# Optimization experiments

Hardware: AMD Instinct MI355X
Metric: run time of the kernel (lower is better)

Reference implementation:

```python
import jax, jax.numpy as jnp
import numpy as np

NUM_HEADS = 4
OUTPUT_DIM = 32
NUM_NODES = 50000
NUM_EDGES = 800000
INPUT_DIM = 128


def setup_inputs() -> dict:
    key = jax.random.key(0)
    k1, k2, k3, k4 = jax.random.split(key, 4)
    node_features = jax.random.uniform(k1, (NUM_NODES, INPUT_DIM), dtype=jnp.float32)
    edge_index = jax.random.randint(k2, (2, NUM_EDGES), 0, NUM_NODES, dtype=jnp.int64)
    # Linear weight (xavier-like scale), stored as [in, out] for x @ W
    W = jax.random.normal(k3, (INPUT_DIM, NUM_HEADS * OUTPUT_DIM), dtype=jnp.float32) * 0.1
    att = jax.random.normal(k4, (2 * OUTPUT_DIM, 1), dtype=jnp.float32) * 0.2
    return {"node_features": node_features, "edge_index": edge_index, "W": W, "att": att}


def reference(node_features, edge_index, W, att):
    num_nodes = node_features.shape[0]
    # Linear projection -> [N, H, D]  (dropout = identity in eval mode)
    proj = (node_features @ W).reshape(num_nodes, NUM_HEADS, OUTPUT_DIM)
    src = proj[edge_index[0]]   # [E, H, D]
    tgt = proj[edge_index[1]]   # [E, H, D]
    # concat([src,tgt]) @ att  ==  src @ att[:D] + tgt @ att[D:]
    a_src = att[:OUTPUT_DIM, 0]   # [D]
    a_tgt = att[OUTPUT_DIM:, 0]   # [D]
    scores = jax.nn.leaky_relu(
        jnp.einsum('ehd,d->eh', src, a_src) + jnp.einsum('ehd,d->eh', tgt, a_tgt),
        negative_slope=0.01,
    )  # [E, H]
    # Faithful to original: softmax over the HEADS axis (dim=-1 of [E, H])
    alpha = jax.nn.softmax(scores, axis=-1)  # [E, H]
    weighted = tgt * alpha[..., None]        # [E, H, D]
    # index_add_ on dim 0 with edge_index[0]
    out = jax.ops.segment_sum(weighted, edge_index[0], num_segments=num_nodes)  # [N, H, D]
    # concat_heads=False -> mean over heads
    return out.mean(axis=1)  # [N, D]
```

## Files before the change

kernel.cpp:

```cpp
#include <hip/hip_runtime.h>
#include <math.h>

#define N_NODES 50000
#define N_EDGES 800000
#define IN_DIM 128
#define N_HEADS 4
#define OUT_DIM 32
#define PROJ_DIM 128
#define WSTR 144

#define NBIN 196
#define BINCAP 5000
#define MAXDEG 64

#define PROJ_BLKS 391
#define PART_BLKS 391
#define FUSE_BLKS (NBIN + PROJ_BLKS)

typedef short bf16x8 __attribute__((ext_vector_type(8)));
typedef float f32x4  __attribute__((ext_vector_type(4)));
typedef _Float16 h2  __attribute__((ext_vector_type(2)));

__device__ __forceinline__ ushort f32_to_bf16(float f) {
    unsigned u = __float_as_uint(f);
    unsigned r = u + 0x7fffu + ((u >> 16) & 1u);
    return (ushort)(r >> 16);
}

__device__ __forceinline__ bf16x8 cvt8(float4 a, float4 b) {
    bf16x8 r;
    r[0] = (short)f32_to_bf16(a.x); r[1] = (short)f32_to_bf16(a.y);
    r[2] = (short)f32_to_bf16(a.z); r[3] = (short)f32_to_bf16(a.w);
    r[4] = (short)f32_to_bf16(b.x); r[5] = (short)f32_to_bf16(b.y);
    r[6] = (short)f32_to_bf16(b.z); r[7] = (short)f32_to_bf16(b.w);
    return r;
}

__device__ __forceinline__ ushort f32_to_f16(float f) {
    return __builtin_bit_cast(ushort, (_Float16)f);
}

__global__ __launch_bounds__(256) void partition_kernel(
    const int* __restrict__ ei, int* __restrict__ bin_cursor,
    unsigned* __restrict__ slab)
{
    __shared__ int cnt[256];
    __shared__ int gbase[256];

    const int tid = threadIdx.x;

    for (int t = tid; t < NBIN; t += 256) cnt[t] = 0;
    __syncthreads();

    const int ebase = blockIdx.x * 2048;
    unsigned srcv[8], tgtv[8];
    int rank[8];
#pragma unroll
    for (int i = 0; i < 8; ++i) {
        int e = ebase + i * 256 + tid;
        bool ok = e < N_EDGES;
        srcv[i] = ok ? (unsigned)ei[e] : 0u;
        tgtv[i] = ok ? (unsigned)ei[N_EDGES + e] : 0u;
        rank[i] = ok ? atomicAdd(&cnt[srcv[i] >> 8], 1) : -1;
    }
    __syncthreads();

    for (int t = tid; t < NBIN; t += 256)
        gbase[t] = atomicAdd(&bin_cursor[t], cnt[t]);
    __syncthreads();

#pragma unroll
    for (int i = 0; i < 8; ++i) {
        if (rank[i] >= 0) {
            int bin = srcv[i] >> 8;
            int p = gbase[bin] + rank[i];
            if (p < BINCAP)
                slab[bin * BINCAP + p] = (tgtv[i] << 16) | (srcv[i] & 255u);
        }
    }
}

__global__ __launch_bounds__(256) void fused_kernel(
    const float* __restrict__ X, const float* __restrict__ W,
    const float* __restrict__ att,
    const unsigned* __restrict__ slab, const int* __restrict__ bin_cursor,
    ushort* __restrict__ projT, float* __restrict__ s_src, float* __restrict__ s_tgt,
    ushort* __restrict__ csr, int* __restrict__ offs, int* __restrict__ deg)
{
    __shared__ ushort Wt[128 * WSTR];

    const int tid = threadIdx.x;

    if (blockIdx.x < NBIN) {
        int*    cnt2 = (int*)Wt;
        int*    ex   = cnt2 + 256;
        int*    wsum = ex + 256;
        ushort* stgt = (ushort*)(wsum + 8);

        const int b = blockIdx.x;
        const int t = tid;
        const int lane = t & 63;
        const int wid  = t >> 6;
        int n_e = bin_cursor[b];
        n_e = (n_e < BINCAP) ? n_e : BINCAP;

        cnt2[t] = 0;
        __syncthreads();

        unsigned pk[20];
        int npk = 0;
        for (int i = t; i < n_e; i += 256) {
            unsigned v = slab[b * BINCAP + i];
            int node8 = v & 255u;
            int r = atomicAdd(&cnt2[node8], 1);
            r = (r < 255) ? r : 255;
            pk[npk++] = (v & 0xFFFF0000u) | ((unsigned)r << 8) | (unsigned)node8;
        }
        __syncthreads();

        const int v = cnt2[t];
        int x = v;
#pragma unroll
        for (int off = 1; off < 64; off <<= 1) {
            int y = __shfl_up(x, off);
            x += (lane >= off) ? y : 0;
        }
        if (lane == 63) wsum[wid] = x;
        __syncthreads();
        int add = 0;
#pragma unroll
        for (int w = 0; w < 4; ++w) add += (w < wid) ? wsum[w] : 0;
        const int myex = x + add - v;
        const int mycnt = v;
        ex[t] = myex;
        __syncthreads();

        for (int j = 0; j < npk; ++j) {
            unsigned pv = pk[j];
            int lpos = ex[pv & 255u] + (int)((pv >> 8) & 255u);
            if (lpos < BINCAP) stgt[lpos] = (ushort)(pv >> 16);
        }
        __syncthreads();

        for (int i = t; i < n_e; i += 256) csr[b * BINCAP + i] = stgt[i];
        int node = b * 256 + t;
        if (node < N_NODES) {
            offs[node] = b * BINCAP + myex;
            deg[node]  = mycnt;
        }
        return;
    }

    for (int idx = tid; idx < 64 * 128; idx += 256) {
        int kp = idx >> 7;
        int c  = idx & 127;
        float w0 = W[(2 * kp) * PROJ_DIM + c];
        float w1 = W[(2 * kp + 1) * PROJ_DIM + c];
        unsigned pr = (unsigned)f32_to_bf16(w0) | ((unsigned)f32_to_bf16(w1) << 16);
        *(unsigned*)&Wt[c * WSTR + 2 * kp] = pr;
    }
    __syncthreads();

    const int wv   = tid >> 6;
    const int lane = tid & 63;
    const int m = lane & 15;
    const int q = lane >> 4;
    const int rbase = (blockIdx.x - NBIN) * 128;

    int arow0 = rbase + wv * 32 + m;
    int arow1 = arow0 + 16;
    arow0 = (arow0 < N_NODES) ? arow0 : N_NODES - 1;
    arow1 = (arow1 < N_NODES) ? arow1 : N_NODES - 1;
    const long long xb0 = (long long)arow0 * IN_DIM;
    const long long xb1 = (long long)arow1 * IN_DIM;

    f32x4 acc[2][8];
#pragma unroll
    for (int rt = 0; rt < 2; ++rt)
#pragma unroll
        for (int ct = 0; ct < 8; ++ct) acc[rt][ct] = (f32x4){0.f, 0.f, 0.f, 0.f};

#pragma unroll
    for (int ks = 0; ks < 4; ++ks) {
        const int k0 = ks * 32 + q * 8;
        float4 a0lo = *(const float4*)&X[xb0 + k0];
        float4 a0hi = *(const float4*)&X[xb0 + k0 + 4];
        float4 a1lo = *(const float4*)&X[xb1 + k0];
        float4 a1hi = *(const float4*)&X[xb1 + k0 + 4];
        bf16x8 afrag0 = cvt8(a0lo, a0hi);
        bf16x8 afrag1 = cvt8(a1lo, a1hi);
#pragma unroll
        for (int ct = 0; ct < 8; ++ct) {
            bf16x8 bfrag = *(const bf16x8*)&Wt[(ct * 16 + m) * WSTR + k0];
            acc[0][ct] = __builtin_amdgcn_mfma_f32_16x16x32_bf16(afrag0, bfrag, acc[0][ct], 0, 0, 0);
            acc[1][ct] = __builtin_amdgcn_mfma_f32_16x16x32_bf16(afrag1, bfrag, acc[1][ct], 0, 0, 0);
        }
    }

    const float as_lo = att[m],      as_hi = att[m + 16];
    const float at_lo = att[32 + m], at_hi = att[48 + m];

#pragma unroll
    for (int rt = 0; rt < 2; ++rt) {
        const int rowb = rbase + wv * 32 + rt * 16 + q * 4;
#pragma unroll
        for (int r = 0; r < 4; ++r) {
            const int row = rowb + r;
            float cl[4], ch[4];
#pragma unroll
            for (int h = 0; h < 4; ++h) {
                cl[h] = acc[rt][2 * h][r];
                ch[h] = acc[rt][2 * h + 1][r];
            }
            if (row < N_NODES) {
                ushort4 plo, phi;
                plo.x = f32_to_f16(cl[0]); plo.y = f32_to_f16(cl[1]);
                plo.z = f32_to_f16(cl[2]); plo.w = f32_to_f16(cl[3]);
                phi.x = f32_to_f16(ch[0]); phi.y = f32_to_f16(ch[1]);
                phi.z = f32_to_f16(ch[2]); phi.w = f32_to_f16(ch[3]);
                *(ushort4*)&projT[(long long)row * PROJ_DIM + m * 4] = plo;
                *(ushort4*)&projT[(long long)row * PROJ_DIM + (m + 16) * 4] = phi;
            }
            float ps[4], pt[4];
#pragma unroll
            for (int h = 0; h < 4; ++h) {
                ps[h] = cl[h] * as_lo + ch[h] * as_hi;
                pt[h] = cl[h] * at_lo + ch[h] * at_hi;
            }
#pragma unroll
            for (int off = 8; off > 0; off >>= 1) {
#pragma unroll
                for (int h = 0; h < 4; ++h) {
                    ps[h] += __shfl_down(ps[h], off, 16);
                    pt[h] += __shfl_down(pt[h], off, 16);
                }
            }
            if (m == 0 && row < N_NODES) {
                *(float4*)&s_src[row * N_HEADS] = make_float4(ps[0], ps[1], ps[2], ps[3]);
                *(float4*)&s_tgt[row * N_HEADS] = make_float4(pt[0], pt[1], pt[2], pt[3]);
            }
        }
    }
}

__global__ __launch_bounds__(256) void gather_kernel(
    const int* __restrict__ deg, const int* __restrict__ offs,
    const ushort* __restrict__ csr,
    const float* __restrict__ s_src, const float* __restrict__ s_tgt,
    const ushort* __restrict__ projT, float* __restrict__ out)
{
    __shared__ uint4 edata[4][MAXDEG];

    const int wv   = threadIdx.x >> 6;
    const int lane = threadIdx.x & 63;
    const int node = blockIdx.x * 4 + wv;

    int n = deg[node];
    n = (n < MAXDEG) ? n : MAXDEG;
    const int o = offs[node];

    uint4 ed = make_uint4(0u, 0u, 0u, 0u);
    if (lane < n) {
        int tgt = csr[o + lane];
        float4 ss = *(const float4*)&s_src[node * N_HEADS];
        float4 st = *(const float4*)&s_tgt[tgt * N_HEADS];

        float sc[4] = { ss.x + st.x, ss.y + st.y, ss.z + st.z, ss.w + st.w };
        float mx = -1e30f;
#pragma unroll
        for (int h = 0; h < 4; ++h) {
            sc[h] = (sc[h] > 0.0f) ? sc[h] : 0.01f * sc[h];
            mx = fmaxf(mx, sc[h]);
        }
        float sum = 0.0f;
#pragma unroll
        for (int h = 0; h < 4; ++h) {
            sc[h] = __expf(sc[h] - mx);
            sum += sc[h];
        }
        float inv = 0.25f / sum;

        h2 a01, a23;
        a01.x = (_Float16)(sc[0] * inv);
        a01.y = (_Float16)(sc[1] * inv);
        a23.x = (_Float16)(sc[2] * inv);
        a23.y = (_Float16)(sc[3] * inv);
        ed.x = (unsigned)tgt;
        ed.y = __builtin_bit_cast(unsigned, a01);
        ed.z = __builtin_bit_cast(unsigned, a23);
    }
    edata[wv][lane] = ed;

    const int d    = lane & 31;
    const int half = lane >> 5;

    float acc0 = 0.0f, acc1 = 0.0f, acc2 = 0.0f, acc3 = 0.0f;

    for (int j = 0; j < n; j += 16) {
        uint4 s[8];
#pragma unroll
        for (int u = 0; u < 8; ++u)
            s[u] = edata[wv][j + 2 * u + half];
        uint2 p[8];
#pragma unroll
        for (int u = 0; u < 8; ++u)
            p[u] = *(const uint2*)&projT[(long long)s[u].x * PROJ_DIM + d * 4];
#pragma unroll
        for (int u = 0; u < 8; ++u) {
            h2 a  = __builtin_bit_cast(h2, s[u].y);
            h2 b  = __builtin_bit_cast(h2, s[u].z);
            h2 lo = __builtin_bit_cast(h2, p[u].x);
            h2 hi = __builtin_bit_cast(h2, p[u].y);
            float* accp = (u & 1) ? ((u & 2) ? &acc3 : &acc1)
                                  : ((u & 2) ? &acc2 : &acc0);
            float tt = *accp;
#if __has_builtin(__builtin_amdgcn_fdot2)
            tt = __builtin_amdgcn_fdot2(a, lo, tt, false);
            tt = __builtin_amdgcn_fdot2(b, hi, tt, false);
#else
            tt = fmaf((float)a.x, (float)lo.x, tt);
            tt = fmaf((float)a.y, (float)lo.y, tt);
            tt = fmaf((float)b.x, (float)hi.x, tt);
            tt = fmaf((float)b.y, (float)hi.y, tt);
#endif
            *accp = tt;
        }
    }

    float acc = (acc0 + acc1) + (acc2 + acc3);
    acc += __shfl_down(acc, 32);
    if (lane < 32) out[node * OUT_DIM + d] = acc;
}

extern "C" void kernel_launch(void* const* d_in, const int* in_sizes, int n_in,
                              void* d_out, int out_size, void* d_ws, size_t ws_size,
                              hipStream_t stream) {
    const float* X   = (const float*)d_in[0];
    const int*   ei  = (const int*)d_in[1];
    const float* W   = (const float*)d_in[2];
    const float* att = (const float*)d_in[3];
    float* out = (float*)d_out;

    char* p = (char*)d_ws;
    ushort* projT   = (ushort*)p;   p += (size_t)N_NODES * PROJ_DIM * 2;
    float* s_src    = (float*)p;    p += (size_t)N_NODES * N_HEADS * 4;
    float* s_tgt    = (float*)p;    p += (size_t)N_NODES * N_HEADS * 4;
    unsigned* slab  = (unsigned*)p; p += (size_t)NBIN * BINCAP * 4;
    ushort* csr     = (ushort*)p;   p += (size_t)NBIN * BINCAP * 2;
    int* offs       = (int*)p;      p += (size_t)N_NODES * 4;
    int* deg        = (int*)p;      p += (size_t)N_NODES * 4;
    int* bin_cursor = (int*)p;      p += 256 * 4;

    (void)hipMemsetAsync(bin_cursor, 0, 256 * sizeof(int), stream);

    partition_kernel<<<PART_BLKS, 256, 0, stream>>>(ei, bin_cursor, slab);

    fused_kernel<<<FUSE_BLKS, 256, 0, stream>>>(
        X, W, att, slab, bin_cursor, projT, s_src, s_tgt, csr, offs, deg);

    gather_kernel<<<N_NODES / 4, 256, 0, stream>>>(
        deg, offs, csr, s_src, s_tgt, projT, out);
}
```

Baseline: 136.3 us.

## Shrink source-node bins from 256 to 64 nodes to spread CSR build

Repartitions edges into 782 bins of 64 source nodes each instead of 196 bins of 256, shrinking per-bin capacity and the per-thread packing buffer. The CSR-build blocks become more numerous and lighter, so the bucketing phase spreads across more CUs and per-block load imbalance shrinks. The local scan drops to a single wave. In exchange, the partition kernel's shared histogram has more bins, so each block issues more global atomics when it reserves bin space. Bin capacity overflow now depends on a tighter bound of 1408 edges per 64 nodes.

```diff
diff --git a/kernel.cpp b/kernel.cpp
--- a/kernel.cpp
+++ b/kernel.cpp
@@ -9,8 +9,8 @@
 #define PROJ_DIM 128
 #define WSTR 144
 
-#define NBIN 196
-#define BINCAP 5000
+#define NBIN 782
+#define BINCAP 1408
 #define MAXDEG 64
 
 #define PROJ_BLKS 391
@@ -44,8 +44,8 @@
     const int* __restrict__ ei, int* __restrict__ bin_cursor,
     unsigned* __restrict__ slab)
 {
-    __shared__ int cnt[256];
-    __shared__ int gbase[256];
+    __shared__ int cnt[NBIN];
+    __shared__ int gbase[NBIN];
 
     const int tid = threadIdx.x;
 
@@ -61,7 +61,7 @@
         bool ok = e < N_EDGES;
         srcv[i] = ok ? (unsigned)ei[e] : 0u;
         tgtv[i] = ok ? (unsigned)ei[N_EDGES + e] : 0u;
-        rank[i] = ok ? atomicAdd(&cnt[srcv[i] >> 8], 1) : -1;
+        rank[i] = ok ? atomicAdd(&cnt[srcv[i] >> 6], 1) : -1;
     }
     __syncthreads();
 
@@ -72,10 +72,10 @@
 #pragma unroll
     for (int i = 0; i < 8; ++i) {
         if (rank[i] >= 0) {
-            int bin = srcv[i] >> 8;
+            int bin = srcv[i] >> 6;
             int p = gbase[bin] + rank[i];
             if (p < BINCAP)
-                slab[bin * BINCAP + p] = (tgtv[i] << 16) | (srcv[i] & 255u);
+                slab[bin * BINCAP + p] = (tgtv[i] << 16) | (srcv[i] & 63u);
         }
     }
 }
@@ -93,60 +93,52 @@
 
     if (blockIdx.x < NBIN) {
         int*    cnt2 = (int*)Wt;
-        int*    ex   = cnt2 + 256;
-        int*    wsum = ex + 256;
-        ushort* stgt = (ushort*)(wsum + 8);
+        int*    ex   = cnt2 + 64;
+        ushort* stgt = (ushort*)(ex + 64);
 
         const int b = blockIdx.x;
         const int t = tid;
-        const int lane = t & 63;
-        const int wid  = t >> 6;
         int n_e = bin_cursor[b];
         n_e = (n_e < BINCAP) ? n_e : BINCAP;
 
-        cnt2[t] = 0;
+        if (t < 64) cnt2[t] = 0;
         __syncthreads();
 
-        unsigned pk[20];
+        unsigned pk[6];
         int npk = 0;
         for (int i = t; i < n_e; i += 256) {
             unsigned v = slab[b * BINCAP + i];
-            int node8 = v & 255u;
-            int r = atomicAdd(&cnt2[node8], 1);
+            int node6 = v & 63u;
+            int r = atomicAdd(&cnt2[node6], 1);
             r = (r < 255) ? r : 255;
-            pk[npk++] = (v & 0xFFFF0000u) | ((unsigned)r << 8) | (unsigned)node8;
+            pk[npk++] = (v & 0xFFFF0000u) | ((unsigned)r << 8) | (unsigned)node6;
         }
         __syncthreads();
 
-        const int v = cnt2[t];
-        int x = v;
-#pragma unroll
-        for (int off = 1; off < 64; off <<= 1) {
-            int y = __shfl_up(x, off);
-            x += (lane >= off) ? y : 0;
-        }
-        if (lane == 63) wsum[wid] = x;
-        __syncthreads();
-        int add = 0;
-#pragma unroll
-        for (int w = 0; w < 4; ++w) add += (w < wid) ? wsum[w] : 0;
-        const int myex = x + add - v;
-        const int mycnt = v;
-        ex[t] = myex;
+        if (t < 64) {
+            int v = cnt2[t];
+            int x = v;
+#pragma unroll
+            for (int off = 1; off < 64; off <<= 1) {
+                int y = __shfl_up(x, off);
+                x += (t >= off) ? y : 0;
+            }
+            ex[t] = x - v;
+        }
         __syncthreads();
 
         for (int j = 0; j < npk; ++j) {
             unsigned pv = pk[j];
-            int lpos = ex[pv & 255u] + (int)((pv >> 8) & 255u);
+            int lpos = ex[pv & 63u] + (int)((pv >> 8) & 255u);
             if (lpos < BINCAP) stgt[lpos] = (ushort)(pv >> 16);
         }
         __syncthreads();
 
         for (int i = t; i < n_e; i += 256) csr[b * BINCAP + i] = stgt[i];
-        int node = b * 256 + t;
-        if (node < N_NODES) {
-            offs[node] = b * BINCAP + myex;
-            deg[node]  = mycnt;
+        int node = b * 64 + t;
+        if (t < 64 && node < N_NODES) {
+            offs[node] = b * BINCAP + ex[t];
+            deg[node]  = cnt2[t];
         }
         return;
     }
@@ -349,9 +341,9 @@
     ushort* csr     = (ushort*)p;   p += (size_t)NBIN * BINCAP * 2;
     int* offs       = (int*)p;      p += (size_t)N_NODES * 4;
     int* deg        = (int*)p;      p += (size_t)N_NODES * 4;
-    int* bin_cursor = (int*)p;      p += 256 * 4;
-
-    (void)hipMemsetAsync(bin_cursor, 0, 256 * sizeof(int), stream);
+    int* bin_cursor = (int*)p;      p += 1024 * 4;
+
+    (void)hipMemsetAsync(bin_cursor, 0, NBIN * sizeof(int), stream);
 
     partition_kernel<<<PART_BLKS, 256, 0, stream>>>(ei, bin_cursor, slab);
 
```

Result: slower. 148.7 us (+9.1%).
